# Kernel tuning notes

Hardware: AMD Instinct MI355X
Metric: run time of the kernel (lower is better)

The kernel has to match this reference:

```python
import jax, jax.numpy as jnp
import numpy as np

C = 256
CQ = C // 8  # query/key channels


def setup_inputs() -> dict:
    key = jax.random.key(0)
    ks = jax.random.split(key, 8)
    B, H, W = 4, 64, 64
    x = jax.random.normal(ks[0], (B, C, H, W), dtype=jnp.float32)
    mask = jax.random.uniform(ks[1], (B, 1, H, W), dtype=jnp.float32)
    # 1x1 conv weights stored as [out_ch, in_ch] (kernel_size=1)
    s = 1.0 / np.sqrt(C)
    Wq = jax.random.uniform(ks[2], (CQ, C), dtype=jnp.float32, minval=-s, maxval=s)
    bq = jax.random.uniform(ks[3], (CQ,), dtype=jnp.float32, minval=-s, maxval=s)
    Wk = jax.random.uniform(ks[4], (CQ, C), dtype=jnp.float32, minval=-s, maxval=s)
    bk = jax.random.uniform(ks[5], (CQ,), dtype=jnp.float32, minval=-s, maxval=s)
    Wv = jax.random.uniform(ks[6], (C, C), dtype=jnp.float32, minval=-s, maxval=s)
    bv = jax.random.uniform(ks[7], (C,), dtype=jnp.float32, minval=-s, maxval=s)
    gamma = jnp.ones((1,), dtype=jnp.float32)
    return {"x": x, "mask": mask, "Wq": Wq, "bq": bq, "Wk": Wk, "bk": bk,
            "Wv": Wv, "bv": bv, "gamma": gamma}


def reference(x, mask, Wq, bq, Wk, bk, Wv, bv, gamma):
    B, Cc, H, W = x.shape
    N = H * W
    xf = x.reshape(B, Cc, N)                  # [B, C, N]
    m = mask.reshape(B, 1, N)                 # [B, 1, N]
    # 1x1 convs == per-pixel linear maps over channels
    q = jnp.einsum('oc,bcn->bon', Wq, xf) + bq[None, :, None]  # [B, CQ, N]
    k = jnp.einsum('oc,bcn->bon', Wk, xf) + bk[None, :, None]  # [B, CQ, N]
    v = jnp.einsum('oc,bcn->bon', Wv, xf) + bv[None, :, None]  # [B, C,  N]
    q = q * m
    k = k * m
    energy = jnp.einsum('bci,bcj->bij', q, k)  # [B, N, N] (queries x keys)
    attn = jax.nn.softmax(energy, axis=-1)
    out = jnp.einsum('bcj,bij->bci', v, attn)  # [B, C, N]
    out = out.reshape(B, Cc, H, W)
    return gamma * out + x
```

## Files before the change

kernel.cpp:

```cpp
#include <hip/hip_runtime.h>
#include <math.h>

#define CC 256
#define NPIX 4096
#define BATCH 4
#define LOG2E 1.4426950408889634f

typedef __attribute__((ext_vector_type(8)))  short short8;
typedef __attribute__((ext_vector_type(16))) float f32x16;

union FragU { short8 v; short s[8]; unsigned u[4]; uint2 d[2]; };
union F8 { uint2 d; long long ll; };

__device__ inline unsigned pkbf(float a, float b) {
    unsigned x = __float_as_uint(a), y = __float_as_uint(b);
    x = (x + 0x7FFFu + ((x >> 16) & 1u)) >> 16;
    y = (y + 0x7FFFu + ((y >> 16) & 1u)) & 0xFFFF0000u;
    return x | y;
}
__device__ inline unsigned short bf1(float a) {
    unsigned x = __float_as_uint(a);
    return (unsigned short)((x + 0x7FFFu + ((x >> 16) & 1u)) >> 16);
}
__device__ inline float ex2(float x) { return __builtin_amdgcn_exp2f(x); }
__device__ inline unsigned pk4fp8(float a, float b, float c, float d) {
    int r = __builtin_amdgcn_cvt_pk_fp8_f32(a, b, 0, false);
    r = __builtin_amdgcn_cvt_pk_fp8_f32(c, d, r, true);
    return (unsigned)r;
}
__device__ inline f32x16 zero16() {
    f32x16 v;
    #pragma unroll
    for (int i = 0; i < 16; ++i) v[i] = 0.0f;
    return v;
}
__device__ inline f32x16 mfma32(short8 a, short8 b, f32x16 c) {
    return __builtin_amdgcn_mfma_f32_32x32x16_bf16(a, b, c, 0, 0, 0);
}
__device__ inline f32x16 mfma_fp8(long long a, long long b, f32x16 c) {
    return __builtin_amdgcn_mfma_f32_32x32x16_fp8_fp8(a, b, c, 0, 0, 0);
}

__global__ __launch_bounds__(256, 2) void prep_kernel(
    const float* __restrict__ x,
    const float* __restrict__ Wq, const float* __restrict__ Wk,
    const float* __restrict__ Wv,
    unsigned short* __restrict__ xT, unsigned short* __restrict__ Wfrag)
{
    const int t = threadIdx.x;
    const int bid = blockIdx.x;
    if (bid < 256) {
        __shared__ unsigned short xs[256 * 68];
        const int b = bid >> 6, u = bid & 63;
        const int p0 = u * 64;
        const float* xb = x + (size_t)b * CC * NPIX + p0;
        #pragma unroll
        for (int k = 0; k < 16; ++k) {
            int c = (t >> 4) + 16 * k;
            int p4 = (t & 15) * 4;
            float4 v = *(const float4*)(xb + (size_t)c * NPIX + p4);
            *(uint2*)&xs[c * 68 + p4] = make_uint2(pkbf(v.x, v.y), pkbf(v.z, v.w));
        }
        __syncthreads();
        const int w = t >> 6, l = t & 63;
        const int c8 = l & 31;
        #pragma unroll
        for (int i = 0; i < 8; ++i) {
            int p = i * 8 + w * 2 + (l >> 5);
            unsigned short tmp[8];
            #pragma unroll
            for (int j = 0; j < 8; ++j) tmp[j] = xs[(c8 * 8 + j) * 68 + p];
            uint4 o;
            o.x = tmp[0] | ((unsigned)tmp[1] << 16);
            o.y = tmp[2] | ((unsigned)tmp[3] << 16);
            o.z = tmp[4] | ((unsigned)tmp[5] << 16);
            o.w = tmp[6] | ((unsigned)tmp[7] << 16);
            *(uint4*)(xT + (size_t)(b * NPIX + p0 + p) * 256 + c8 * 8) = o;
        }
    } else {
        const int wb = bid - 256;
        const int l = t & 63, rr = t >> 6;
        #pragma unroll
        for (int e = 0; e < 4; ++e) {
            int gs = wb * 4 + e;
            int g = gs >> 4, s = gs & 15;
            const float* src; float scale = 1.0f; int oc0 = 0;
            if (g == 0)      { src = Wq; scale = LOG2E; }
            else if (g == 1) { src = Wk; }
            else             { src = Wv; oc0 = (g - 2) * 32; }
            int row = oc0 + (l & 31);
            int kb2 = 16 * s + 8 * (l >> 5) + rr * 2;
            float v0 = src[(size_t)row * CC + kb2] * scale;
            float v1 = src[(size_t)row * CC + kb2 + 1] * scale;
            *(unsigned*)(Wfrag + (size_t)(gs * 64 + l) * 8 + rr * 2) = pkbf(v0, v1);
        }
    }
}

__global__ __launch_bounds__(320, 3) void proj_mfma(
    const unsigned short* __restrict__ xT, const unsigned short* __restrict__ Wfrag,
    const float* __restrict__ mask,
    const float* __restrict__ bq, const float* __restrict__ bk,
    const float* __restrict__ bv,
    unsigned short* __restrict__ qT, unsigned short* __restrict__ kT,
    unsigned char* __restrict__ vI)
{
    __shared__ unsigned short xls[64 * 260];
    const int t = threadIdx.x;
    const int w = t >> 6, l = t & 63, L = l & 31, h = l >> 5;
    const int bid = blockIdx.x;
    const int b    = (bid >> 1) & 3;
    const int u    = ((bid >> 3) << 1) | (bid & 1);
    const int p0   = (u >> 1) * 64;
    const int half = u & 1;
    const int ocg  = half * 5 + w;

    const unsigned short* xg = xT + (size_t)(b * NPIX + p0) * 256;
    #pragma unroll
    for (int r = 0; r < 7; ++r) {
        int idx = r * 2560 + t * 8;
        if (idx < 16384) {
            uint4 d = *(const uint4*)(xg + idx);
            int p = idx >> 8, c = idx & 255;
            *(uint2*)&xls[p * 260 + c]     = make_uint2(d.x, d.y);
            *(uint2*)&xls[p * 260 + c + 4] = make_uint2(d.z, d.w);
        }
    }

    FragU wf[16];
    const unsigned short* wp = Wfrag + (size_t)(ocg * 16 * 64 + l) * 8;
    #pragma unroll
    for (int s = 0; s < 16; ++s) wf[s].v = *(const short8*)(wp + s * 512);

    float bcol;
    if (ocg == 0)      bcol = bq[L] * LOG2E;
    else if (ocg == 1) bcol = bk[L];
    else               bcol = bv[(ocg - 2) * 32 + L];
    const float* mb = mask + (size_t)b * NPIX;
    __syncthreads();

    #pragma unroll
    for (int mt = 0; mt < 2; ++mt) {
        const int pp = 32 * mt;
        f32x16 acc = zero16();
        #pragma unroll
        for (int s = 0; s < 16; ++s) {
            FragU af;
            const unsigned short* ap = &xls[(pp + L) * 260 + 16 * s + 8 * h];
            af.d[0] = *(const uint2*)(ap);
            af.d[1] = *(const uint2*)(ap + 4);
            acc = mfma32(af.v, wf[s].v, acc);
        }
        if (ocg < 2) {
            unsigned short* dst = (ocg ? kT : qT) + (size_t)b * NPIX * 32;
            #pragma unroll
            for (int r = 0; r < 16; ++r) {
                int prow = (r & 3) + 8 * (r >> 2) + 4 * h;
                float mv = mb[p0 + pp + prow];
                dst[(size_t)(p0 + pp + prow) * 32 + L] = bf1((acc[r] + bcol) * mv);
            }
        } else {
            const int cg = ocg - 2;
            unsigned char* vbp = vI + (size_t)(b * 8 + cg) * 512 * 32 * 8;
            #pragma unroll
            for (int m = 0; m < 4; ++m) {
                int jo = ((p0 + pp) >> 3) + m;
                unsigned pk = pk4fp8(acc[4*m]   + bcol, acc[4*m+1] + bcol,
                                     acc[4*m+2] + bcol, acc[4*m+3] + bcol);
                *(unsigned*)(vbp + (((size_t)jo * 32 + L) * 8 + 4 * h)) = pk;
            }
        }
    }
}

__global__ __launch_bounds__(256, 2) void attn_mfma(
    const unsigned short* __restrict__ qT, const unsigned short* __restrict__ kT,
    const unsigned char* __restrict__ vI, const float* __restrict__ x,
    const float* __restrict__ gamma, float* __restrict__ out)
{
    __shared__ float mls[2][4][32];
    __shared__ float obuf[4][2048];

    const int t = threadIdx.x;
    const int w = t >> 6, l = t & 63, L = l & 31, h = l >> 5;
    const int bid = blockIdx.x;
    const int b  = (bid >> 1) & 3;
    const int it = (bid >> 3) * 2 + (bid & 1);
    const int i0 = it * 32;

    const unsigned short* qrow = qT + ((size_t)b * NPIX + i0 + L) * 32 + 8 * h;
    short8 qf0 = *(const short8*)(qrow);
    short8 qf1 = *(const short8*)(qrow + 16);

    const unsigned short* kb = kT + (size_t)b * NPIX * 32;
    const unsigned char* vb = vI + (size_t)b * 8 * 512 * 32 * 8;

    f32x16 acc[8];
    #pragma unroll
    for (int cg = 0; cg < 8; ++cg) acc[cg] = zero16();
    float m_run = -INFINITY, l_run = 0.0f;

    const int jbase = w * 1024;
    const unsigned short* kr0 = kb + (size_t)(jbase + L) * 32 + 8 * h;
    short8 ka0 = *(const short8*)(kr0);
    short8 ka1 = *(const short8*)(kr0 + 16);
    short8 kb0 = *(const short8*)(kr0 + 1024);
    short8 kb1 = *(const short8*)(kr0 + 1024 + 16);

    for (int itr = 0; itr < 16; ++itr) {
        const int j0 = jbase + itr * 64;

        f32x16 s0 = zero16(), s1 = zero16();
        s0 = mfma32(ka0, qf0, s0);
        s0 = mfma32(ka1, qf1, s0);
        s1 = mfma32(kb0, qf0, s1);
        s1 = mfma32(kb1, qf1, s1);

        if (itr < 15) {
            const unsigned short* kr = kb + (size_t)(j0 + 64 + L) * 32 + 8 * h;
            ka0 = *(const short8*)(kr);
            ka1 = *(const short8*)(kr + 16);
            kb0 = *(const short8*)(kr + 1024);
            kb1 = *(const short8*)(kr + 1024 + 16);
        }
        F8 vA[8], vB[8];
        {
            const size_t c0 = (size_t)(j0 >> 3) + h;
            #pragma unroll
            for (int cg = 0; cg < 8; ++cg) {
                vA[cg].d = *(const uint2*)(vb + (((size_t)cg * 512 + c0) * 32 + L) * 8);
                vB[cg].d = *(const uint2*)(vb + (((size_t)cg * 512 + c0 + 2) * 32 + L) * 8);
            }
        }

        float tmax = s0[0];
        #pragma unroll
        for (int r = 1; r < 16; ++r) tmax = fmaxf(tmax, s0[r]);
        #pragma unroll
        for (int r = 0; r < 16; ++r) tmax = fmaxf(tmax, s1[r]);
        tmax = fmaxf(tmax, __shfl_xor(tmax, 32));
        float m_new = fmaxf(m_run, tmax);
        if (__ballot(tmax > m_run)) {
            float alpha = ex2(m_run - m_new);
            l_run *= alpha;
            #pragma unroll
            for (int cg = 0; cg < 8; ++cg)
                #pragma unroll
                for (int r = 0; r < 16; ++r) acc[cg][r] *= alpha;
        }
        m_run = m_new;

        float ssum = 0.0f;
        #pragma unroll
        for (int r = 0; r < 16; ++r) { s0[r] = ex2(s0[r] - m_new); ssum += s0[r]; }
        #pragma unroll
        for (int r = 0; r < 16; ++r) { s1[r] = ex2(s1[r] - m_new); ssum += s1[r]; }
        ssum += __shfl_xor(ssum, 32);
        l_run += ssum;

        unsigned ua8[4], ub8[4], pa8[4], pb8[4];
        #pragma unroll
        for (int m = 0; m < 4; ++m) {
            ua8[m] = pk4fp8(s0[4*m], s0[4*m+1], s0[4*m+2], s0[4*m+3]);
            ub8[m] = pk4fp8(s1[4*m], s1[4*m+1], s1[4*m+2], s1[4*m+3]);
        }
        #pragma unroll
        for (int q = 0; q < 4; ++q) {
            pa8[q] = (unsigned)__shfl_xor((int)ua8[q], 32);
            pb8[q] = (unsigned)__shfl_xor((int)ub8[q], 32);
        }

        F8 vcur[8], pf;
        #pragma unroll
        for (int cg = 0; cg < 8; ++cg) vcur[cg] = vA[cg];
        {
            const size_t jox = (size_t)(j0 >> 3) + 4 + h;
            #pragma unroll
            for (int cg = 0; cg < 8; ++cg)
                vA[cg].d = *(const uint2*)(vb + (((size_t)cg * 512 + jox) * 32 + L) * 8);
        }
        pf.d.x = h ? pa8[1] : ua8[0];
        pf.d.y = h ? ua8[1] : pa8[0];
        #pragma unroll
        for (int cg = 0; cg < 8; ++cg) acc[cg] = mfma_fp8(vcur[cg].ll, pf.ll, acc[cg]);
        #pragma unroll
        for (int cg = 0; cg < 8; ++cg) vcur[cg] = vB[cg];
        {
            const size_t jox = (size_t)(j0 >> 3) + 6 + h;
            #pragma unroll
            for (int cg = 0; cg < 8; ++cg)
                vB[cg].d = *(const uint2*)(vb + (((size_t)cg * 512 + jox) * 32 + L) * 8);
        }
        pf.d.x = h ? pa8[3] : ua8[2];
        pf.d.y = h ? ua8[3] : pa8[2];
        #pragma unroll
        for (int cg = 0; cg < 8; ++cg) acc[cg] = mfma_fp8(vcur[cg].ll, pf.ll, acc[cg]);
        pf.d.x = h ? pb8[1] : ub8[0];
        pf.d.y = h ? ub8[1] : pb8[0];
        #pragma unroll
        for (int cg = 0; cg < 8; ++cg) acc[cg] = mfma_fp8(vA[cg].ll, pf.ll, acc[cg]);
        pf.d.x = h ? pb8[3] : ub8[2];
        pf.d.y = h ? ub8[3] : pb8[2];
        #pragma unroll
        for (int cg = 0; cg < 8; ++cg) acc[cg] = mfma_fp8(vB[cg].ll, pf.ll, acc[cg]);
    }

    if (h == 0) { mls[0][w][L] = m_run; mls[1][w][L] = l_run; }
    __syncthreads();
    float m0 = mls[0][0][L], m1 = mls[0][1][L], m2 = mls[0][2][L], m3 = mls[0][3][L];
    float ms = fmaxf(fmaxf(m0, m1), fmaxf(m2, m3));
    float f0 = ex2(m0 - ms), f1 = ex2(m1 - ms);
    float f2 = ex2(m2 - ms), f3 = ex2(m3 - ms);
    float lstar = f0 * mls[1][0][L] + f1 * mls[1][1][L]
                + f2 * mls[1][2][L] + f3 * mls[1][3][L];
    float fw = (w == 0) ? f0 : (w == 1) ? f1 : (w == 2) ? f2 : f3;
    const float scale = gamma[0] / lstar;

    #pragma unroll
    for (int cg = 0; cg < 8; ++cg)
        #pragma unroll
        for (int r = 0; r < 16; ++r) acc[cg][r] *= fw;

    const int ti = t & 31, trow = t >> 5;
    for (int ck = 0; ck < 4; ++ck) {
        #pragma unroll
        for (int half = 0; half < 2; ++half) {
            #pragma unroll
            for (int r = 0; r < 16; ++r) {
                int prow = (r & 3) + 8 * (r >> 2) + 4 * h;
                obuf[w][half * 1024 + prow * 32 + L] = acc[2 * ck + half][r];
            }
        }
        __syncthreads();
        #pragma unroll
        for (int rr = 0; rr < 8; ++rr) {
            int cr = trow + 8 * rr;
            int idx = cr * 32 + ti;
            float sum = obuf[0][idx] + obuf[1][idx] + obuf[2][idx] + obuf[3][idx];
            size_t gi = ((size_t)b * CC + ck * 64 + cr) * NPIX + i0 + ti;
            out[gi] = scale * sum + x[gi];
        }
        __syncthreads();
    }
}

extern "C" void kernel_launch(void* const* d_in, const int* in_sizes, int n_in,
                              void* d_out, int out_size, void* d_ws, size_t ws_size,
                              hipStream_t stream) {
    const float* x     = (const float*)d_in[0];
    const float* mask  = (const float*)d_in[1];
    const float* Wq    = (const float*)d_in[2];
    const float* bq    = (const float*)d_in[3];
    const float* Wk    = (const float*)d_in[4];
    const float* bk    = (const float*)d_in[5];
    const float* Wv    = (const float*)d_in[6];
    const float* bv    = (const float*)d_in[7];
    const float* gamma = (const float*)d_in[8];
    float* out = (float*)d_out;

    unsigned short* ws = (unsigned short*)d_ws;
    unsigned short* qT = ws;
    unsigned short* kT = qT + (size_t)BATCH * NPIX * 32;
    unsigned char*  vI = (unsigned char*)(kT + (size_t)BATCH * NPIX * 32);
    unsigned short* xT = (unsigned short*)(vI + (size_t)BATCH * CC * NPIX);
    unsigned short* Wfrag = xT + (size_t)BATCH * NPIX * 256;

    prep_kernel<<<296, 256, 0, stream>>>(x, Wq, Wk, Wv, xT, Wfrag);
    proj_mfma<<<512, 320, 0, stream>>>(xT, Wfrag, mask, bq, bk, bv, qT, kT, vI);
    attn_mfma<<<512, 256, 0, stream>>>(qT, kT, vI, x, gamma, out);
}
```

Before: 146.3 us.

## Interleave V fp8 layout per lane, use pointer-increment loads, lazy softmax rescale

The V projection output is re-laid out so each lane's eight channel-group fragments for a 16-key slab are contiguous 64-byte chunks, which turns scattered 8-byte loads into sequential per-lane reads. K and V loads in the attention loop now use running byte pointers instead of recomputed indices, and the K prefetch is unconditional, so the last iteration reads past the wave's range. The online softmax only rescales when the new max exceeds the running max by more than 3 (log2 units), which skips most accumulator rescaling. The trade-off is that unnormalised exponentials can reach up to 2^3, which adds some overflow/precision risk in the fp8 P values.

```diff
diff --git a/kernel.cpp b/kernel.cpp
--- a/kernel.cpp
+++ b/kernel.cpp
@@ -161,13 +161,15 @@
             }
         } else {
             const int cg = ocg - 2;
-            unsigned char* vbp = vI + (size_t)(b * 8 + cg) * 512 * 32 * 8;
+            unsigned char* vbp = vI + (size_t)b * (256 * 4096);
+            const int jsb = (p0 + pp) >> 4;
             #pragma unroll
             for (int m = 0; m < 4; ++m) {
-                int jo = ((p0 + pp) >> 3) + m;
+                int js = jsb + (m >> 1);
+                int lanep = (m & 1) * 32 + L;
                 unsigned pk = pk4fp8(acc[4*m]   + bcol, acc[4*m+1] + bcol,
                                      acc[4*m+2] + bcol, acc[4*m+3] + bcol);
-                *(unsigned*)(vbp + (((size_t)jo * 32 + L) * 8 + 4 * h)) = pk;
+                *(unsigned*)(vbp + (size_t)(js * 64 + lanep) * 64 + cg * 8 + 4 * h) = pk;
             }
         }
     }
@@ -192,46 +194,42 @@
     short8 qf0 = *(const short8*)(qrow);
     short8 qf1 = *(const short8*)(qrow + 16);
 
-    const unsigned short* kb = kT + (size_t)b * NPIX * 32;
-    const unsigned char* vb = vI + (size_t)b * 8 * 512 * 32 * 8;
+    const int jbase = w * 1024;
+    const unsigned char* kp = (const unsigned char*)kT
+        + (size_t)b * NPIX * 64 + (size_t)jbase * 64 + (size_t)L * 64 + 16 * h;
+    short8 ka0 = *(const short8*)(kp);
+    short8 ka1 = *(const short8*)(kp + 32);
+    short8 kb0 = *(const short8*)(kp + 2048);
+    short8 kb1 = *(const short8*)(kp + 2080);
+    kp += 4096;
+    const unsigned char* vp = vI + (size_t)b * (256 * 4096)
+        + (size_t)(jbase >> 4) * 4096 + (size_t)l * 64;
 
     f32x16 acc[8];
     #pragma unroll
     for (int cg = 0; cg < 8; ++cg) acc[cg] = zero16();
     float m_run = -INFINITY, l_run = 0.0f;
 
-    const int jbase = w * 1024;
-    const unsigned short* kr0 = kb + (size_t)(jbase + L) * 32 + 8 * h;
-    short8 ka0 = *(const short8*)(kr0);
-    short8 ka1 = *(const short8*)(kr0 + 16);
-    short8 kb0 = *(const short8*)(kr0 + 1024);
-    short8 kb1 = *(const short8*)(kr0 + 1024 + 16);
-
     for (int itr = 0; itr < 16; ++itr) {
-        const int j0 = jbase + itr * 64;
-
         f32x16 s0 = zero16(), s1 = zero16();
         s0 = mfma32(ka0, qf0, s0);
         s0 = mfma32(ka1, qf1, s0);
         s1 = mfma32(kb0, qf0, s1);
         s1 = mfma32(kb1, qf1, s1);
 
-        if (itr < 15) {
-            const unsigned short* kr = kb + (size_t)(j0 + 64 + L) * 32 + 8 * h;
-            ka0 = *(const short8*)(kr);
-            ka1 = *(const short8*)(kr + 16);
-            kb0 = *(const short8*)(kr + 1024);
-            kb1 = *(const short8*)(kr + 1024 + 16);
-        }
+        ka0 = *(const short8*)(kp);
+        ka1 = *(const short8*)(kp + 32);
+        kb0 = *(const short8*)(kp + 2048);
+        kb1 = *(const short8*)(kp + 2080);
+        kp += 4096;
+
         F8 vA[8], vB[8];
-        {
-            const size_t c0 = (size_t)(j0 >> 3) + h;
-            #pragma unroll
-            for (int cg = 0; cg < 8; ++cg) {
-                vA[cg].d = *(const uint2*)(vb + (((size_t)cg * 512 + c0) * 32 + L) * 8);
-                vB[cg].d = *(const uint2*)(vb + (((size_t)cg * 512 + c0 + 2) * 32 + L) * 8);
-            }
-        }
+        #pragma unroll
+        for (int cg = 0; cg < 8; ++cg) vA[cg].d = *(const uint2*)(vp + cg * 8);
+        vp += 4096;
+        #pragma unroll
+        for (int cg = 0; cg < 8; ++cg) vB[cg].d = *(const uint2*)(vp + cg * 8);
+        vp += 4096;
 
         float tmax = s0[0];
         #pragma unroll
@@ -239,22 +237,22 @@
         #pragma unroll
         for (int r = 0; r < 16; ++r) tmax = fmaxf(tmax, s1[r]);
         tmax = fmaxf(tmax, __shfl_xor(tmax, 32));
-        float m_new = fmaxf(m_run, tmax);
-        if (__ballot(tmax > m_run)) {
+        if (__ballot(tmax > m_run + 3.0f)) {
+            float m_new = fmaxf(m_run, tmax);
             float alpha = ex2(m_run - m_new);
             l_run *= alpha;
             #pragma unroll
             for (int cg = 0; cg < 8; ++cg)
                 #pragma unroll
                 for (int r = 0; r < 16; ++r) acc[cg][r] *= alpha;
-        }
-        m_run = m_new;
+            m_run = m_new;
+        }
 
         float ssum = 0.0f;
         #pragma unroll
-        for (int r = 0; r < 16; ++r) { s0[r] = ex2(s0[r] - m_new); ssum += s0[r]; }
-        #pragma unroll
-        for (int r = 0; r < 16; ++r) { s1[r] = ex2(s1[r] - m_new); ssum += s1[r]; }
+        for (int r = 0; r < 16; ++r) { s0[r] = ex2(s0[r] - m_run); ssum += s0[r]; }
+        #pragma unroll
+        for (int r = 0; r < 16; ++r) { s1[r] = ex2(s1[r] - m_run); ssum += s1[r]; }
         ssum += __shfl_xor(ssum, 32);
         l_run += ssum;
 
@@ -273,24 +271,18 @@
         F8 vcur[8], pf;
         #pragma unroll
         for (int cg = 0; cg < 8; ++cg) vcur[cg] = vA[cg];
-        {
-            const size_t jox = (size_t)(j0 >> 3) + 4 + h;
-            #pragma unroll
-            for (int cg = 0; cg < 8; ++cg)
-                vA[cg].d = *(const uint2*)(vb + (((size_t)cg * 512 + jox) * 32 + L) * 8);
-        }
+        #pragma unroll
+        for (int cg = 0; cg < 8; ++cg) vA[cg].d = *(const uint2*)(vp + cg * 8);
+        vp += 4096;
         pf.d.x = h ? pa8[1] : ua8[0];
         pf.d.y = h ? ua8[1] : pa8[0];
         #pragma unroll
         for (int cg = 0; cg < 8; ++cg) acc[cg] = mfma_fp8(vcur[cg].ll, pf.ll, acc[cg]);
         #pragma unroll
         for (int cg = 0; cg < 8; ++cg) vcur[cg] = vB[cg];
-        {
-            const size_t jox = (size_t)(j0 >> 3) + 6 + h;
-            #pragma unroll
-            for (int cg = 0; cg < 8; ++cg)
-                vB[cg].d = *(const uint2*)(vb + (((size_t)cg * 512 + jox) * 32 + L) * 8);
-        }
+        #pragma unroll
+        for (int cg = 0; cg < 8; ++cg) vB[cg].d = *(const uint2*)(vp + cg * 8);
+        vp += 4096;
         pf.d.x = h ? pa8[3] : ua8[2];
         pf.d.y = h ? ua8[3] : pa8[2];
         #pragma unroll
```

Result: no change. 145.5 us (-0.6%).
